# Kernel optimization log

Measured on AMD Instinct MI355X. Metric: run time of the kernel, lower is better.

Reference implementation:

```python
import jax, jax.numpy as jnp
import numpy as np

B, T, D, H = 4, 2048, 1024, 16
DH = D // H  # head dim = 64
FLOAT_MIN = jnp.finfo(jnp.float32).min


def setup_inputs() -> dict:
    key = jax.random.key(0)
    k1, k2, k3 = jax.random.split(key, 3)
    scale = 1.0 / np.sqrt(D)
    return {
        "x": jax.random.normal(k1, (B, T, D), dtype=jnp.float32),
        "W_qkv": jax.random.normal(k2, (D, 3 * D), dtype=jnp.float32) * scale,
        "b_qkv": jnp.zeros((3 * D,), dtype=jnp.float32),
        "W_out": jax.random.normal(k3, (D, D), dtype=jnp.float32) * scale,
        "b_out": jnp.zeros((D,), dtype=jnp.float32),
        "mask": jnp.ones((B, T, T), dtype=jnp.float32),
    }


def _split_heads(t):
    # [B, T, D] -> [B, H, T, DH]
    b, s, _ = t.shape
    return t.reshape(b, s, H, DH).transpose(0, 2, 1, 3)


def reference(x, W_qkv, b_qkv, W_out, b_out, mask):
    # fused QKV projection (Conv1D kernel-size 1 == per-position dense)
    qkv = jnp.einsum("btd,de->bte", x, W_qkv) + b_qkv
    q, k, v = jnp.split(qkv, 3, axis=-1)
    q = _split_heads(q) * (DH ** -0.5)  # [B, H, T, DH]
    k = _split_heads(k)
    v = _split_heads(v)
    # scores [B, H, Tq, Tk]
    dot = jnp.einsum("bhqd,bhkd->bhqk", q, k)
    m = mask[:, None, :, :]  # expand over heads
    dot = dot * m + (1.0 - m) * FLOAT_MIN
    attn = jax.nn.softmax(dot, axis=-1)
    ctx = jnp.einsum("bhqk,bhkd->bhqd", attn, v)  # [B, H, T, DH]
    combined = ctx.transpose(0, 2, 1, 3).reshape(x.shape[0], x.shape[1], D)
    out = jnp.einsum("btd,de->bte", combined, W_out) + b_out
    return out
```

## Files before the change

### kernel.cpp

```cpp
#include <hip/hip_runtime.h>

typedef short bf16x8 __attribute__((ext_vector_type(8)));
typedef float f32x4 __attribute__((ext_vector_type(4)));
typedef float f32x16 __attribute__((ext_vector_type(16)));
typedef unsigned short u16x8 __attribute__((ext_vector_type(8)));

#define DEVI __device__ __forceinline__

static constexpr int T_ = 2048;

DEVI unsigned short f2bf(float f) {
  unsigned int x = __builtin_bit_cast(unsigned int, f);
  x += 0x7fffu + ((x >> 16) & 1u);
  return (unsigned short)(x >> 16);
}

DEVI unsigned int cvtpk(float lo, float hi2) {
  unsigned int r;
  asm("v_cvt_pk_bf16_f32 %0, %1, %2" : "=v"(r) : "v"(lo), "v"(hi2));
  return r;
}

DEVI float exp2_raw(float x) {
  float r;
  asm("v_exp_f32 %0, %1" : "=v"(r) : "v"(x));
  return r;
}

DEVI int swz23(int r) {
  const int d = ((r >> 2) ^ (r >> 3)) & 1;
  return r ^ (d << 2) ^ (d << 3);
}

DEVI bf16x8 mkfrag(unsigned a, unsigned b, unsigned c, unsigned d) {
  union { unsigned u[4]; bf16x8 v; } x;
  x.u[0] = a; x.u[1] = b; x.u[2] = c; x.u[3] = d;
  return x.v;
}

DEVI void gl2lds16(const void* g, const void* l) {
  __builtin_amdgcn_global_load_lds(
      (const __attribute__((address_space(1))) void*)g,
      (__attribute__((address_space(3))) void*)l, 16, 0, 0);
}

__global__ __launch_bounds__(256) void k_cvt_bf16(const float* __restrict__ in,
                                                  unsigned short* __restrict__ out) {
  size_t i = ((size_t)blockIdx.x * 256 + threadIdx.x) * 8;
  float4 a = *(const float4*)(in + i);
  float4 b = *(const float4*)(in + i + 4);
  u16x8 o;
  o[0] = f2bf(a.x); o[1] = f2bf(a.y); o[2] = f2bf(a.z); o[3] = f2bf(a.w);
  o[4] = f2bf(b.x); o[5] = f2bf(b.y); o[6] = f2bf(b.z); o[7] = f2bf(b.w);
  *(u16x8*)(out + i) = o;
}

__global__ __launch_bounds__(256) void k_mask_scan(const uint4* __restrict__ m,
                                                   unsigned int* __restrict__ flag) {
  const unsigned int ONE = 0x3f800000u;
  size_t i0 = ((size_t)blockIdx.x * 256 + threadIdx.x) * 8;
  bool ok = true;
#pragma unroll
  for (int i = 0; i < 8; ++i) {
    uint4 v = m[i0 + i];
    ok &= (v.x == ONE) & (v.y == ONE) & (v.z == ONE) & (v.w == ONE);
  }
  if (!ok) atomicAnd(flag, 0u);
}

template <int R, int C>
__global__ __launch_bounds__(256) void k_transpose_cvt(const float* __restrict__ in,
                                                       unsigned short* __restrict__ out) {
  __shared__ unsigned short t[64][65];
  const int c0 = blockIdx.x * 64, r0 = blockIdx.y * 64;
  const int cc = threadIdx.x & 63, r4 = threadIdx.x >> 6;
#pragma unroll
  for (int i = 0; i < 16; ++i) {
    int rr = i * 4 + r4;
    t[rr][cc] = f2bf(in[(size_t)(r0 + rr) * C + c0 + cc]);
  }
  __syncthreads();
#pragma unroll
  for (int i = 0; i < 16; ++i) {
    int rr = i * 4 + r4;
    out[(size_t)(c0 + rr) * R + r0 + cc] = t[cc][rr];
  }
}

__global__ __launch_bounds__(256) void k_transpose_v(const unsigned short* __restrict__ V,
                                                     unsigned short* __restrict__ Vt) {
  __shared__ unsigned short t[64][65];
  const int t0 = blockIdx.x * 64;
  const size_t bh = blockIdx.y;
  const unsigned short* src = V + (bh * T_ + t0) * 64;
  unsigned short* dst = Vt + bh * 64 * T_ + t0;
  const int cc = threadIdx.x & 63, r4 = threadIdx.x >> 6;
#pragma unroll
  for (int i = 0; i < 16; ++i) {
    int rr = i * 4 + r4;
    t[rr][cc] = src[(size_t)rr * 64 + cc];
  }
  __syncthreads();
#pragma unroll
  for (int i = 0; i < 16; ++i) {
    int rr = i * 4 + r4;
    dst[(size_t)rr * T_ + cc] = t[cc][rr];
  }
}

template <int EPI>
__global__ __launch_bounds__(256, 3) void k_gemm(
    const unsigned short* __restrict__ A, const unsigned short* __restrict__ Bt,
    const float* __restrict__ bias,
    unsigned short* __restrict__ qo, unsigned short* __restrict__ ko2,
    unsigned short* __restrict__ vo, float* __restrict__ fo) {
  __shared__ unsigned short As[2][128 * 32];
  __shared__ unsigned short Bs[2][128 * 32];
  const int tid = threadIdx.x;
  const int lane = tid & 63, w = tid >> 6;
  const int wr = w >> 1, wc = w & 1;
  const int g = lane >> 4, c0 = lane & 15;
  const int m0 = blockIdx.y * 128, n0 = blockIdx.x * 128;

  f32x4 acc[4][4] = {};

  const int s0 = tid, s1 = tid + 256;
  const int ar0 = s0 >> 2, ac0 = (s0 & 3) ^ ((ar0 >> 1) & 3);
  const int ar1 = s1 >> 2, ac1 = (s1 & 3) ^ ((ar1 >> 1) & 3);
  const int ldsb0 = w * 512, ldsb1 = w * 512 + 2048;

  const unsigned short* Ar0 = A + (size_t)(m0 + ar0) * 1024 + ac0 * 8;
  const unsigned short* Ar1 = A + (size_t)(m0 + ar1) * 1024 + ac1 * 8;
  const unsigned short* Br0 = Bt + (size_t)(n0 + ar0) * 1024 + ac0 * 8;
  const unsigned short* Br1 = Bt + (size_t)(n0 + ar1) * 1024 + ac1 * 8;

  auto stage = [&](int buf, int kt) {
    const int ke = kt * 32;
    gl2lds16(Ar0 + ke, &As[buf][ldsb0]);
    gl2lds16(Ar1 + ke, &As[buf][ldsb1]);
    gl2lds16(Br0 + ke, &Bs[buf][ldsb0]);
    gl2lds16(Br1 + ke, &Bs[buf][ldsb1]);
  };

  stage(0, 0);
  __syncthreads();
  int cur = 0;
  for (int kt = 0; kt < 32; ++kt) {
    if (kt + 1 < 32) stage(cur ^ 1, kt + 1);
    bf16x8 af[4], bfv[4];
#pragma unroll
    for (int mf = 0; mf < 4; ++mf) {
      int row = wr * 64 + mf * 16 + c0;
      int ch = g ^ ((row >> 1) & 3);
      af[mf] = *(const bf16x8*)&As[cur][row * 32 + ch * 8];
    }
#pragma unroll
    for (int nf = 0; nf < 4; ++nf) {
      int row = wc * 64 + nf * 16 + c0;
      int ch = g ^ ((row >> 1) & 3);
      bfv[nf] = *(const bf16x8*)&Bs[cur][row * 32 + ch * 8];
    }
    __builtin_amdgcn_s_setprio(1);
#pragma unroll
    for (int mf = 0; mf < 4; ++mf)
#pragma unroll
      for (int nf = 0; nf < 4; ++nf)
        acc[mf][nf] = __builtin_amdgcn_mfma_f32_16x16x32_bf16(af[mf], bfv[nf], acc[mf][nf], 0, 0, 0);
    __builtin_amdgcn_s_setprio(0);
    __syncthreads();
    cur ^= 1;
  }

#pragma unroll
  for (int mf = 0; mf < 4; ++mf) {
#pragma unroll
    for (int nf = 0; nf < 4; ++nf) {
      const int n = n0 + wc * 64 + nf * 16 + c0;
      const float bv = bias[n];
#pragma unroll
      for (int r = 0; r < 4; ++r) {
        const int m = m0 + wr * 64 + mf * 16 + g * 4 + r;
        float v = acc[mf][nf][r] + bv;
        if constexpr (EPI == 0) {
          const int sel = n >> 10, hd = n & 1023;
          const int h = hd >> 6, d = hd & 63;
          const int b = m >> 11, t = m & 2047;
          const size_t off = ((size_t)((b * 16 + h) * 2048 + t)) * 64 + d;
          if (sel == 0)       qo[off] = f2bf(v * 0.125f);
          else if (sel == 1)  ko2[off] = f2bf(v);
          else                vo[off] = f2bf(v);
        } else {
          fo[(size_t)m * 1024 + n] = v;
        }
      }
    }
  }
}

__global__ __launch_bounds__(256, 4) void k_attn(
    const unsigned short* __restrict__ Q, const unsigned short* __restrict__ Kg_,
    const unsigned short* __restrict__ Vt, const float* __restrict__ mask,
    const unsigned int* __restrict__ maskflag,
    unsigned short* __restrict__ ctx) {
  __shared__ unsigned short Ks[2][64 * 64];
  __shared__ unsigned short Vs[2][64 * 64];
  const int tid = threadIdx.x, lane = tid & 63, w = tid >> 6;
  const int q = lane & 31, hi = lane >> 5;

  const int flat = blockIdx.x + 16 * blockIdx.y + 256 * blockIdx.z;
  const int work = (flat & 7) * 128 + (flat >> 3);
  const int qb = work & 15;
  const int bh_i = work >> 4;
  const int h = bh_i & 15, b = bh_i >> 4;
  const int t0 = qb * 128;
  const size_t bh = (size_t)bh_i;

  const unsigned short* Qg = Q + (bh * 2048 + t0 + w * 32 + q) * 64;
  const unsigned short* Kg = Kg_ + bh * 2048 * 64;
  const unsigned short* Vg = Vt + bh * 64 * 2048;
  const float* Mg = mask + (size_t)b * 2048 * 2048;
  const bool allones = (*maskflag != 0u);

  bf16x8 qf[4];
#pragma unroll
  for (int kd = 0; kd < 4; ++kd)
    qf[kd] = *(const bf16x8*)(Qg + kd * 16 + hi * 8);

  f32x16 ot[2] = {};
  float mrun = -__builtin_inff(), lrun = 0.f;

  const int s0 = tid, s1 = tid + 256;
  const int kr0 = s0 >> 3, kc0 = (s0 & 7) ^ (kr0 & 7);
  const int kr1 = s1 >> 3, kc1 = (s1 & 7) ^ (kr1 & 7);
  const int kp0 = swz23(kr0), kp1 = swz23(kr1);
  const int ldsb0 = w * 512, ldsb1 = w * 512 + 2048;

  auto stageKV = [&](int buf, int kt) {
    gl2lds16(Kg + (size_t)(kt * 64 + kp0) * 64 + kc0 * 8, &Ks[buf][ldsb0]);
    gl2lds16(Kg + (size_t)(kt * 64 + kp1) * 64 + kc1 * 8, &Ks[buf][ldsb1]);
    gl2lds16(Vg + (size_t)kr0 * 2048 + kt * 64 + kc0 * 8, &Vs[buf][ldsb0]);
    gl2lds16(Vg + (size_t)kr1 * 2048 + kt * 64 + kc1 * 8, &Vs[buf][ldsb1]);
  };

  stageKV(0, 0);
  __syncthreads();
  int cur = 0;
  const float MINF = -3.402823466e38f;
  const float L2E = 1.4426950408889634f;

  for (int kt = 0; kt < 32; ++kt) {
    if (kt + 1 < 32) stageKV(cur ^ 1, kt + 1);

    f32x16 st[2] = {};
#pragma unroll
    for (int mt2 = 0; mt2 < 2; ++mt2) {
      __builtin_amdgcn_s_setprio(1);
#pragma unroll
      for (int kd = 0; kd < 4; ++kd) {
        const int row = mt2 * 32 + q;
        const int ch = (2 * kd + hi) ^ (row & 7);
        bf16x8 kf = *(const bf16x8*)&Ks[cur][row * 64 + ch * 8];
        st[mt2] = __builtin_amdgcn_mfma_f32_32x32x16_bf16(kf, qf[kd], st[mt2], 0, 0, 0);
      }
      __builtin_amdgcn_s_setprio(0);
    }

    if (!allones) {
      const int qg = t0 + w * 32 + q;
#pragma unroll
      for (int mt2 = 0; mt2 < 2; ++mt2)
#pragma unroll
        for (int r = 0; r < 16; ++r) {
          const int kg = kt * 64 + mt2 * 32 +
                         (r & 3) + 4 * ((r >> 2) & 1) + 8 * hi + 16 * (r >> 3);
          const float mv = Mg[(size_t)qg * 2048 + kg];
          st[mt2][r] = st[mt2][r] * mv + (1.f - mv) * MINF;
        }
    }

    float g4[8];
#pragma unroll
    for (int i = 0; i < 4; ++i) {
      g4[i]     = fmaxf(fmaxf(fmaxf(st[0][4 * i], st[0][4 * i + 1]), st[0][4 * i + 2]), st[0][4 * i + 3]);
      g4[i + 4] = fmaxf(fmaxf(fmaxf(st[1][4 * i], st[1][4 * i + 1]), st[1][4 * i + 2]), st[1][4 * i + 3]);
    }
    float r1 = fmaxf(fmaxf(g4[0], g4[1]), g4[2]);
    float r2 = fmaxf(fmaxf(g4[3], g4[4]), g4[5]);
    float r3 = fmaxf(fmaxf(g4[6], g4[7]), r1);
    float tmax = fmaxf(r2, r3);
    tmax = fmaxf(tmax, __shfl_xor(tmax, 32));
    const bool defer = (__all(tmax <= mrun + 8.f) != 0);
    float alpha = 1.f;
    if (!defer) {
      const float mnew = fmaxf(mrun, tmax);
      alpha = exp2_raw((mrun - mnew) * L2E);
      mrun = mnew;
    }
    const float mL2 = mrun * L2E;
#pragma unroll
    for (int mt2 = 0; mt2 < 2; ++mt2)
#pragma unroll
      for (int i = 0; i < 16; ++i)
        st[mt2][i] = exp2_raw(st[mt2][i] * L2E - mL2);
    float s8[8];
#pragma unroll
    for (int i = 0; i < 8; ++i)
      s8[i] = (st[0][i] + st[0][i + 8]) + (st[1][i] + st[1][i + 8]);
    float s4a = s8[0] + s8[4], s4b = s8[1] + s8[5];
    float s4c = s8[2] + s8[6], s4d = s8[3] + s8[7];
    float ps = (s4a + s4b) + (s4c + s4d);
    ps += __shfl_xor(ps, 32);
    lrun = lrun * alpha + ps;
    if (!defer) {
#pragma unroll
      for (int dt = 0; dt < 2; ++dt)
#pragma unroll
        for (int i = 0; i < 16; ++i) ot[dt][i] *= alpha;
    }

    bf16x8 pf[4];
#pragma unroll
    for (int mt2 = 0; mt2 < 2; ++mt2) {
      unsigned int pw[8];
#pragma unroll
      for (int i = 0; i < 8; ++i) pw[i] = cvtpk(st[mt2][2 * i], st[mt2][2 * i + 1]);
      pf[2 * mt2]     = mkfrag(pw[0], pw[1], pw[2], pw[3]);
      pf[2 * mt2 + 1] = mkfrag(pw[4], pw[5], pw[6], pw[7]);
    }

#pragma unroll
    for (int dt = 0; dt < 2; ++dt) {
      __builtin_amdgcn_s_setprio(1);
#pragma unroll
      for (int kt2 = 0; kt2 < 4; ++kt2) {
        const int row = dt * 32 + q;
        const int ch = (2 * kt2 + hi) ^ (row & 7);
        bf16x8 vf = *(const bf16x8*)&Vs[cur][row * 64 + ch * 8];
        ot[dt] = __builtin_amdgcn_mfma_f32_32x32x16_bf16(vf, pf[kt2], ot[dt], 0, 0, 0);
      }
      __builtin_amdgcn_s_setprio(0);
    }

    __syncthreads();
    cur ^= 1;
  }

  const int qg = t0 + w * 32 + q;
  const float rl = 1.f / lrun;
  unsigned short* cp = ctx + ((size_t)b * 2048 + qg) * 1024 + h * 64;
#pragma unroll
  for (int dt = 0; dt < 2; ++dt) {
#pragma unroll
    for (int rg = 0; rg < 4; ++rg) {
      const int d0 = dt * 32 + rg * 8 + hi * 4;
      ushort4 o;
      o.x = f2bf(ot[dt][rg * 4 + 0] * rl);
      o.y = f2bf(ot[dt][rg * 4 + 1] * rl);
      o.z = f2bf(ot[dt][rg * 4 + 2] * rl);
      o.w = f2bf(ot[dt][rg * 4 + 3] * rl);
      *(ushort4*)(cp + d0) = o;
    }
  }
}

extern "C" void kernel_launch(void* const* d_in, const int* in_sizes, int n_in,
                              void* d_out, int out_size, void* d_ws, size_t ws_size,
                              hipStream_t stream) {
  (void)in_sizes; (void)n_in; (void)out_size; (void)ws_size;
  const float* x    = (const float*)d_in[0];
  const float* Wqkv = (const float*)d_in[1];
  const float* bqkv = (const float*)d_in[2];
  const float* Wout = (const float*)d_in[3];
  const float* bout = (const float*)d_in[4];
  const float* mask = (const float*)d_in[5];
  float* out = (float*)d_out;
  char* ws = (char*)d_ws;

  const size_t SZ_BTD = (size_t)8192 * 1024 * 2;
  unsigned short* xb  = (unsigned short*)(ws);
  unsigned short* Wqt = (unsigned short*)(ws + SZ_BTD);
  unsigned short* Wot = (unsigned short*)(ws + SZ_BTD + 6291456);
  unsigned short* Qb  = (unsigned short*)(ws + SZ_BTD + 8388608);
  unsigned short* Kb  = (unsigned short*)(ws + SZ_BTD + 8388608 + SZ_BTD);
  unsigned short* Vb  = (unsigned short*)(ws + SZ_BTD + 8388608 + 2 * SZ_BTD);
  unsigned short* Vtb = (unsigned short*)(ws + SZ_BTD + 8388608 + 3 * SZ_BTD);
  unsigned int* flag  = (unsigned int*)(ws + SZ_BTD + 8388608 + 4 * SZ_BTD);
  unsigned short* ctx = xb;

  hipMemsetAsync(flag, 1, 4, stream);
  k_mask_scan<<<2048, 256, 0, stream>>>((const uint4*)mask, flag);
  k_cvt_bf16<<<4096, 256, 0, stream>>>(x, xb);
  k_transpose_cvt<1024, 3072><<<dim3(48, 16), 256, 0, stream>>>(Wqkv, Wqt);
  k_transpose_cvt<1024, 1024><<<dim3(16, 16), 256, 0, stream>>>(Wout, Wot);
  k_gemm<0><<<dim3(24, 64), 256, 0, stream>>>(xb, Wqt, bqkv, Qb, Kb, Vb, nullptr);
  k_transpose_v<<<dim3(32, 64), 256, 0, stream>>>(Vb, Vtb);
  k_attn<<<dim3(16, 16, 4), 256, 0, stream>>>(Qb, Kb, Vtb, mask, flag, ctx);
  k_gemm<1><<<dim3(8, 64), 256, 0, stream>>>(ctx, Wot, bout, nullptr, nullptr, nullptr, out);
}
```

Baseline: 230.8 us.

## Process two query tiles per wave in attention to reuse K/V fragments

Each attention wave now handles 64 query rows, as two 32-row sub-tiles sharing every K and V fragment read from LDS. The block size grows to 256 queries and the grid shrinks to 512 blocks. Launch bounds are lowered to 2 blocks per CU to make room for the doubled accumulators. Separately, the GEMM drops its MFMA priority boosts and lowers its occupancy bound. The goal is to halve LDS reads and global K/V staging per query, at the cost of lower occupancy and fewer blocks across the CUs.

```diff
diff --git a/kernel.cpp b/kernel.cpp
--- a/kernel.cpp
+++ b/kernel.cpp
@@ -109,7 +109,7 @@
 }
 
 template <int EPI>
-__global__ __launch_bounds__(256, 3) void k_gemm(
+__global__ __launch_bounds__(256, 2) void k_gemm(
     const unsigned short* __restrict__ A, const unsigned short* __restrict__ Bt,
     const float* __restrict__ bias,
     unsigned short* __restrict__ qo, unsigned short* __restrict__ ko2,
@@ -160,13 +160,11 @@
       int ch = g ^ ((row >> 1) & 3);
       bfv[nf] = *(const bf16x8*)&Bs[cur][row * 32 + ch * 8];
     }
-    __builtin_amdgcn_s_setprio(1);
 #pragma unroll
     for (int mf = 0; mf < 4; ++mf)
 #pragma unroll
       for (int nf = 0; nf < 4; ++nf)
         acc[mf][nf] = __builtin_amdgcn_mfma_f32_16x16x32_bf16(af[mf], bfv[nf], acc[mf][nf], 0, 0, 0);
-    __builtin_amdgcn_s_setprio(0);
     __syncthreads();
     cur ^= 1;
   }
@@ -197,7 +195,7 @@
   }
 }
 
-__global__ __launch_bounds__(256, 4) void k_attn(
+__global__ __launch_bounds__(256, 2) void k_attn(
     const unsigned short* __restrict__ Q, const unsigned short* __restrict__ Kg_,
     const unsigned short* __restrict__ Vt, const float* __restrict__ mask,
     const unsigned int* __restrict__ maskflag,
@@ -207,27 +205,31 @@
   const int tid = threadIdx.x, lane = tid & 63, w = tid >> 6;
   const int q = lane & 31, hi = lane >> 5;
 
-  const int flat = blockIdx.x + 16 * blockIdx.y + 256 * blockIdx.z;
-  const int work = (flat & 7) * 128 + (flat >> 3);
-  const int qb = work & 15;
-  const int bh_i = work >> 4;
+  const int flat = blockIdx.x;
+  const int work = (flat & 7) * 64 + (flat >> 3);
+  const int qb = work & 7;
+  const int bh_i = work >> 3;
   const int h = bh_i & 15, b = bh_i >> 4;
-  const int t0 = qb * 128;
+  const int t0 = qb * 256;
   const size_t bh = (size_t)bh_i;
 
-  const unsigned short* Qg = Q + (bh * 2048 + t0 + w * 32 + q) * 64;
+  const unsigned short* Qg0 = Q + (bh * 2048 + t0 + w * 64 + q) * 64;
+  const unsigned short* Qg1 = Qg0 + 32 * 64;
   const unsigned short* Kg = Kg_ + bh * 2048 * 64;
   const unsigned short* Vg = Vt + bh * 64 * 2048;
   const float* Mg = mask + (size_t)b * 2048 * 2048;
   const bool allones = (*maskflag != 0u);
 
-  bf16x8 qf[4];
-#pragma unroll
-  for (int kd = 0; kd < 4; ++kd)
-    qf[kd] = *(const bf16x8*)(Qg + kd * 16 + hi * 8);
-
-  f32x16 ot[2] = {};
-  float mrun = -__builtin_inff(), lrun = 0.f;
+  bf16x8 qf0[4], qf1[4];
+#pragma unroll
+  for (int kd = 0; kd < 4; ++kd) {
+    qf0[kd] = *(const bf16x8*)(Qg0 + kd * 16 + hi * 8);
+    qf1[kd] = *(const bf16x8*)(Qg1 + kd * 16 + hi * 8);
+  }
+
+  f32x16 ot0[2] = {}, ot1[2] = {};
+  float mrun0 = -__builtin_inff(), lrun0 = 0.f;
+  float mrun1 = -__builtin_inff(), lrun1 = 0.f;
 
   const int s0 = tid, s1 = tid + 256;
   const int kr0 = s0 >> 3, kc0 = (s0 & 7) ^ (kr0 & 7);
@@ -248,36 +250,7 @@
   const float MINF = -3.402823466e38f;
   const float L2E = 1.4426950408889634f;
 
-  for (int kt = 0; kt < 32; ++kt) {
-    if (kt + 1 < 32) stageKV(cur ^ 1, kt + 1);
-
-    f32x16 st[2] = {};
-#pragma unroll
-    for (int mt2 = 0; mt2 < 2; ++mt2) {
-      __builtin_amdgcn_s_setprio(1);
-#pragma unroll
-      for (int kd = 0; kd < 4; ++kd) {
-        const int row = mt2 * 32 + q;
-        const int ch = (2 * kd + hi) ^ (row & 7);
-        bf16x8 kf = *(const bf16x8*)&Ks[cur][row * 64 + ch * 8];
-        st[mt2] = __builtin_amdgcn_mfma_f32_32x32x16_bf16(kf, qf[kd], st[mt2], 0, 0, 0);
-      }
-      __builtin_amdgcn_s_setprio(0);
-    }
-
-    if (!allones) {
-      const int qg = t0 + w * 32 + q;
-#pragma unroll
-      for (int mt2 = 0; mt2 < 2; ++mt2)
-#pragma unroll
-        for (int r = 0; r < 16; ++r) {
-          const int kg = kt * 64 + mt2 * 32 +
-                         (r & 3) + 4 * ((r >> 2) & 1) + 8 * hi + 16 * (r >> 3);
-          const float mv = Mg[(size_t)qg * 2048 + kg];
-          st[mt2][r] = st[mt2][r] * mv + (1.f - mv) * MINF;
-        }
-    }
-
+  auto softmax_pack = [&](f32x16* st, float& mrun, float& lrun, f32x16* ot, bf16x8* pf) {
     float g4[8];
 #pragma unroll
     for (int i = 0; i < 4; ++i) {
@@ -317,8 +290,6 @@
 #pragma unroll
         for (int i = 0; i < 16; ++i) ot[dt][i] *= alpha;
     }
-
-    bf16x8 pf[4];
 #pragma unroll
     for (int mt2 = 0; mt2 < 2; ++mt2) {
       unsigned int pw[8];
@@ -327,6 +298,44 @@
       pf[2 * mt2]     = mkfrag(pw[0], pw[1], pw[2], pw[3]);
       pf[2 * mt2 + 1] = mkfrag(pw[4], pw[5], pw[6], pw[7]);
     }
+  };
+
+  for (int kt = 0; kt < 32; ++kt) {
+    if (kt + 1 < 32) stageKV(cur ^ 1, kt + 1);
+
+    f32x16 st0[2] = {}, st1[2] = {};
+#pragma unroll
+    for (int mt2 = 0; mt2 < 2; ++mt2) {
+      __builtin_amdgcn_s_setprio(1);
+#pragma unroll
+      for (int kd = 0; kd < 4; ++kd) {
+        const int row = mt2 * 32 + q;
+        const int ch = (2 * kd + hi) ^ (row & 7);
+        bf16x8 kf = *(const bf16x8*)&Ks[cur][row * 64 + ch * 8];
+        st0[mt2] = __builtin_amdgcn_mfma_f32_32x32x16_bf16(kf, qf0[kd], st0[mt2], 0, 0, 0);
+        st1[mt2] = __builtin_amdgcn_mfma_f32_32x32x16_bf16(kf, qf1[kd], st1[mt2], 0, 0, 0);
+      }
+      __builtin_amdgcn_s_setprio(0);
+    }
+
+    if (!allones) {
+      const int qg0 = t0 + w * 64 + q;
+#pragma unroll
+      for (int mt2 = 0; mt2 < 2; ++mt2)
+#pragma unroll
+        for (int r = 0; r < 16; ++r) {
+          const int kg = kt * 64 + mt2 * 32 +
+                         (r & 3) + 4 * ((r >> 2) & 1) + 8 * hi + 16 * (r >> 3);
+          const float mv0 = Mg[(size_t)qg0 * 2048 + kg];
+          const float mv1 = Mg[(size_t)(qg0 + 32) * 2048 + kg];
+          st0[mt2][r] = st0[mt2][r] * mv0 + (1.f - mv0) * MINF;
+          st1[mt2][r] = st1[mt2][r] * mv1 + (1.f - mv1) * MINF;
+        }
+    }
+
+    bf16x8 pf0[4], pf1[4];
+    softmax_pack(st0, mrun0, lrun0, ot0, pf0);
+    softmax_pack(st1, mrun1, lrun1, ot1, pf1);
 
 #pragma unroll
     for (int dt = 0; dt < 2; ++dt) {
@@ -336,7 +345,8 @@
         const int row = dt * 32 + q;
         const int ch = (2 * kt2 + hi) ^ (row & 7);
         bf16x8 vf = *(const bf16x8*)&Vs[cur][row * 64 + ch * 8];
-        ot[dt] = __builtin_amdgcn_mfma_f32_32x32x16_bf16(vf, pf[kt2], ot[dt], 0, 0, 0);
+        ot0[dt] = __builtin_amdgcn_mfma_f32_32x32x16_bf16(vf, pf0[kt2], ot0[dt], 0, 0, 0);
+        ot1[dt] = __builtin_amdgcn_mfma_f32_32x32x16_bf16(vf, pf1[kt2], ot1[dt], 0, 0, 0);
       }
       __builtin_amdgcn_s_setprio(0);
     }
@@ -345,20 +355,26 @@
     cur ^= 1;
   }
 
-  const int qg = t0 + w * 32 + q;
-  const float rl = 1.f / lrun;
-  unsigned short* cp = ctx + ((size_t)b * 2048 + qg) * 1024 + h * 64;
+  const int qg0 = t0 + w * 64 + q;
+  const float rl0 = 1.f / lrun0, rl1 = 1.f / lrun1;
+  unsigned short* cp0 = ctx + ((size_t)b * 2048 + qg0) * 1024 + h * 64;
+  unsigned short* cp1 = cp0 + (size_t)32 * 1024;
 #pragma unroll
   for (int dt = 0; dt < 2; ++dt) {
 #pragma unroll
     for (int rg = 0; rg < 4; ++rg) {
       const int d0 = dt * 32 + rg * 8 + hi * 4;
-      ushort4 o;
-      o.x = f2bf(ot[dt][rg * 4 + 0] * rl);
-      o.y = f2bf(ot[dt][rg * 4 + 1] * rl);
-      o.z = f2bf(ot[dt][rg * 4 + 2] * rl);
-      o.w = f2bf(ot[dt][rg * 4 + 3] * rl);
-      *(ushort4*)(cp + d0) = o;
+      ushort4 o0, o1;
+      o0.x = f2bf(ot0[dt][rg * 4 + 0] * rl0);
+      o0.y = f2bf(ot0[dt][rg * 4 + 1] * rl0);
+      o0.z = f2bf(ot0[dt][rg * 4 + 2] * rl0);
+      o0.w = f2bf(ot0[dt][rg * 4 + 3] * rl0);
+      o1.x = f2bf(ot1[dt][rg * 4 + 0] * rl1);
+      o1.y = f2bf(ot1[dt][rg * 4 + 1] * rl1);
+      o1.z = f2bf(ot1[dt][rg * 4 + 2] * rl1);
+      o1.w = f2bf(ot1[dt][rg * 4 + 3] * rl1);
+      *(ushort4*)(cp0 + d0) = o0;
+      *(ushort4*)(cp1 + d0) = o1;
     }
   }
 }
@@ -394,6 +410,6 @@
   k_transpose_cvt<1024, 1024><<<dim3(16, 16), 256, 0, stream>>>(Wout, Wot);
   k_gemm<0><<<dim3(24, 64), 256, 0, stream>>>(xb, Wqt, bqkv, Qb, Kb, Vb, nullptr);
   k_transpose_v<<<dim3(32, 64), 256, 0, stream>>>(Vb, Vtb);
-  k_attn<<<dim3(16, 16, 4), 256, 0, stream>>>(Qb, Kb, Vtb, mask, flag, ctx);
+  k_attn<<<512, 256, 0, stream>>>(Qb, Kb, Vtb, mask, flag, ctx);
   k_gemm<1><<<dim3(8, 64), 256, 0, stream>>>(ctx, Wot, bout, nullptr, nullptr, nullptr, out);
 }
```

After: 239.9 us. 4.0% more time.

## Fuse V transpose into QKV GEMM epilogue and remap blocks across XCDs

Applied to the files above, without the earlier changes.

The QKV GEMM epilogue now writes V directly in transposed [B,H,DH,T] layout, so the separate V-transpose kernel and its intermediate buffer are removed. Block indices are remapped so consecutive blocks are spread across the 8 XCD chunks, which is meant to improve L2 locality. The change also drops the s_setprio hints around the MFMA loop and lowers the launch-bounds occupancy hint from 3 to 2. The transposed V stores are strided (2048 elements apart per d), so the epilogue writes become poorly coalesced.

```diff
diff --git a/kernel.cpp b/kernel.cpp
--- a/kernel.cpp
+++ b/kernel.cpp
@@ -87,40 +87,24 @@
   }
 }
 
-__global__ __launch_bounds__(256) void k_transpose_v(const unsigned short* __restrict__ V,
-                                                     unsigned short* __restrict__ Vt) {
-  __shared__ unsigned short t[64][65];
-  const int t0 = blockIdx.x * 64;
-  const size_t bh = blockIdx.y;
-  const unsigned short* src = V + (bh * T_ + t0) * 64;
-  unsigned short* dst = Vt + bh * 64 * T_ + t0;
-  const int cc = threadIdx.x & 63, r4 = threadIdx.x >> 6;
-#pragma unroll
-  for (int i = 0; i < 16; ++i) {
-    int rr = i * 4 + r4;
-    t[rr][cc] = src[(size_t)rr * 64 + cc];
-  }
-  __syncthreads();
-#pragma unroll
-  for (int i = 0; i < 16; ++i) {
-    int rr = i * 4 + r4;
-    dst[(size_t)rr * T_ + cc] = t[cc][rr];
-  }
-}
-
 template <int EPI>
-__global__ __launch_bounds__(256, 3) void k_gemm(
+__global__ __launch_bounds__(256, 2) void k_gemm(
     const unsigned short* __restrict__ A, const unsigned short* __restrict__ Bt,
     const float* __restrict__ bias,
     unsigned short* __restrict__ qo, unsigned short* __restrict__ ko2,
-    unsigned short* __restrict__ vo, float* __restrict__ fo) {
+    unsigned short* __restrict__ vt, float* __restrict__ fo) {
   __shared__ unsigned short As[2][128 * 32];
   __shared__ unsigned short Bs[2][128 * 32];
   const int tid = threadIdx.x;
   const int lane = tid & 63, w = tid >> 6;
   const int wr = w >> 1, wc = w & 1;
   const int g = lane >> 4, c0 = lane & 15;
-  const int m0 = blockIdx.y * 128, n0 = blockIdx.x * 128;
+
+  const int nx = gridDim.x;
+  const int flat = blockIdx.y * nx + blockIdx.x;
+  const int chunk = (nx * gridDim.y) >> 3;
+  const int work = (flat & 7) * chunk + (flat >> 3);
+  const int m0 = (work / nx) * 128, n0 = (work % nx) * 128;
 
   f32x4 acc[4][4] = {};
 
@@ -160,13 +144,11 @@
       int ch = g ^ ((row >> 1) & 3);
       bfv[nf] = *(const bf16x8*)&Bs[cur][row * 32 + ch * 8];
     }
-    __builtin_amdgcn_s_setprio(1);
 #pragma unroll
     for (int mf = 0; mf < 4; ++mf)
 #pragma unroll
       for (int nf = 0; nf < 4; ++nf)
         acc[mf][nf] = __builtin_amdgcn_mfma_f32_16x16x32_bf16(af[mf], bfv[nf], acc[mf][nf], 0, 0, 0);
-    __builtin_amdgcn_s_setprio(0);
     __syncthreads();
     cur ^= 1;
   }
@@ -185,10 +167,10 @@
           const int sel = n >> 10, hd = n & 1023;
           const int h = hd >> 6, d = hd & 63;
           const int b = m >> 11, t = m & 2047;
-          const size_t off = ((size_t)((b * 16 + h) * 2048 + t)) * 64 + d;
-          if (sel == 0)       qo[off] = f2bf(v * 0.125f);
-          else if (sel == 1)  ko2[off] = f2bf(v);
-          else                vo[off] = f2bf(v);
+          const size_t bh = (size_t)(b * 16 + h);
+          if (sel == 0)       qo[(bh * 2048 + t) * 64 + d] = f2bf(v * 0.125f);
+          else if (sel == 1)  ko2[(bh * 2048 + t) * 64 + d] = f2bf(v);
+          else                vt[(bh * 64 + d) * 2048 + t] = f2bf(v);
         } else {
           fo[(size_t)m * 1024 + n] = v;
         }
@@ -382,9 +364,8 @@
   unsigned short* Wot = (unsigned short*)(ws + SZ_BTD + 6291456);
   unsigned short* Qb  = (unsigned short*)(ws + SZ_BTD + 8388608);
   unsigned short* Kb  = (unsigned short*)(ws + SZ_BTD + 8388608 + SZ_BTD);
-  unsigned short* Vb  = (unsigned short*)(ws + SZ_BTD + 8388608 + 2 * SZ_BTD);
-  unsigned short* Vtb = (unsigned short*)(ws + SZ_BTD + 8388608 + 3 * SZ_BTD);
-  unsigned int* flag  = (unsigned int*)(ws + SZ_BTD + 8388608 + 4 * SZ_BTD);
+  unsigned short* Vtb = (unsigned short*)(ws + SZ_BTD + 8388608 + 2 * SZ_BTD);
+  unsigned int* flag  = (unsigned int*)(ws + SZ_BTD + 8388608 + 3 * SZ_BTD);
   unsigned short* ctx = xb;
 
   hipMemsetAsync(flag, 1, 4, stream);
@@ -392,8 +373,7 @@
   k_cvt_bf16<<<4096, 256, 0, stream>>>(x, xb);
   k_transpose_cvt<1024, 3072><<<dim3(48, 16), 256, 0, stream>>>(Wqkv, Wqt);
   k_transpose_cvt<1024, 1024><<<dim3(16, 16), 256, 0, stream>>>(Wout, Wot);
-  k_gemm<0><<<dim3(24, 64), 256, 0, stream>>>(xb, Wqt, bqkv, Qb, Kb, Vb, nullptr);
-  k_transpose_v<<<dim3(32, 64), 256, 0, stream>>>(Vb, Vtb);
+  k_gemm<0><<<dim3(24, 64), 256, 0, stream>>>(xb, Wqt, bqkv, Qb, Kb, Vtb, nullptr);
   k_attn<<<dim3(16, 16, 4), 256, 0, stream>>>(Qb, Kb, Vtb, mask, flag, ctx);
   k_gemm<1><<<dim3(8, 64), 256, 0, stream>>>(ctx, Wot, bout, nullptr, nullptr, nullptr, out);
 }
```

After: 239.0 us. 1.04x slower.

## Rewrite GEMMs with 256x128 tiles, 8 waves, triple-buffered K=64 stages

Applied to the files above, without the earlier changes.

Replaces the 128x128, 4-wave, double-buffered GEMM with a 256x128 tile computed by 8 waves, K-step 64 and a three-deep LDS ring that prefetches two stages ahead under explicit vmcnt waits. A flattened grid remaps blocks so that consecutive workgroups land on different XCDs for better L2 locality. This aims to raise arithmetic intensity per LDS load and hide global latency better. In exchange it uses far more LDS (about 144KB per block), which limits occupancy and makes the hand-placed barrier and waitcnt sequencing fragile.

```diff
diff --git a/kernel.cpp b/kernel.cpp
--- a/kernel.cpp
+++ b/kernel.cpp
@@ -108,78 +108,98 @@
   }
 }
 
-template <int EPI>
-__global__ __launch_bounds__(256, 3) void k_gemm(
+template <int EPI, int NT>
+__global__ __launch_bounds__(512, 2) void k_gemm8(
     const unsigned short* __restrict__ A, const unsigned short* __restrict__ Bt,
     const float* __restrict__ bias,
     unsigned short* __restrict__ qo, unsigned short* __restrict__ ko2,
     unsigned short* __restrict__ vo, float* __restrict__ fo) {
-  __shared__ unsigned short As[2][128 * 32];
-  __shared__ unsigned short Bs[2][128 * 32];
-  const int tid = threadIdx.x;
-  const int lane = tid & 63, w = tid >> 6;
-  const int wr = w >> 1, wc = w & 1;
+  __shared__ unsigned short As[3][256 * 64];
+  __shared__ unsigned short Bs[3][128 * 64];
+  const int tid = threadIdx.x, lane = tid & 63, w = tid >> 6;
+  const int wm = w >> 1, wn = w & 1;
   const int g = lane >> 4, c0 = lane & 15;
-  const int m0 = blockIdx.y * 128, n0 = blockIdx.x * 128;
+
+  const int flat = blockIdx.x;
+  const int work = (flat & 7) * ((32 * NT) >> 3) + (flat >> 3);
+  const int m0 = (work / NT) * 256, n0 = (work % NT) * 128;
 
   f32x4 acc[4][4] = {};
 
-  const int s0 = tid, s1 = tid + 256;
-  const int ar0 = s0 >> 2, ac0 = (s0 & 3) ^ ((ar0 >> 1) & 3);
-  const int ar1 = s1 >> 2, ac1 = (s1 & 3) ^ ((ar1 >> 1) & 3);
-  const int ldsb0 = w * 512, ldsb1 = w * 512 + 2048;
-
-  const unsigned short* Ar0 = A + (size_t)(m0 + ar0) * 1024 + ac0 * 8;
-  const unsigned short* Ar1 = A + (size_t)(m0 + ar1) * 1024 + ac1 * 8;
-  const unsigned short* Br0 = Bt + (size_t)(n0 + ar0) * 1024 + ac0 * 8;
-  const unsigned short* Br1 = Bt + (size_t)(n0 + ar1) * 1024 + ac1 * 8;
-
-  auto stage = [&](int buf, int kt) {
-    const int ke = kt * 32;
-    gl2lds16(Ar0 + ke, &As[buf][ldsb0]);
-    gl2lds16(Ar1 + ke, &As[buf][ldsb1]);
-    gl2lds16(Br0 + ke, &Bs[buf][ldsb0]);
-    gl2lds16(Br1 + ke, &Bs[buf][ldsb1]);
+  const int rs = tid >> 3, chs = tid & 7;
+  const int lwb = w * 512;
+
+  auto stageK = [&](int buf, int kt) {
+    const unsigned short* sa = A + (size_t)m0 * 1024 + kt * 64;
+    const unsigned short* sb = Bt + (size_t)n0 * 1024 + kt * 64;
+    unsigned short* da = &As[buf][0];
+    unsigned short* db = &Bs[buf][0];
+#pragma unroll
+    for (int j = 0; j < 4; ++j) {
+      const int row = rs + j * 64;
+      const int ch = chs ^ (row & 7);
+      gl2lds16(sa + (size_t)row * 1024 + ch * 8, da + j * 4096 + lwb);
+    }
+#pragma unroll
+    for (int j = 0; j < 2; ++j) {
+      const int row = rs + j * 64;
+      const int ch = chs ^ (row & 7);
+      gl2lds16(sb + (size_t)row * 1024 + ch * 8, db + j * 4096 + lwb);
+    }
   };
 
-  stage(0, 0);
-  __syncthreads();
-  int cur = 0;
-  for (int kt = 0; kt < 32; ++kt) {
-    if (kt + 1 < 32) stage(cur ^ 1, kt + 1);
-    bf16x8 af[4], bfv[4];
+  stageK(0, 0);
+  stageK(1, 1);
+  asm volatile("s_waitcnt vmcnt(6)" ::: "memory");
+  __builtin_amdgcn_s_barrier();
+
+  int cb = 0;
+  for (int k = 0; k < 16; ++k) {
+    bf16x8 af[4][2], bfv[4][2];
 #pragma unroll
     for (int mf = 0; mf < 4; ++mf) {
-      int row = wr * 64 + mf * 16 + c0;
-      int ch = g ^ ((row >> 1) & 3);
-      af[mf] = *(const bf16x8*)&As[cur][row * 32 + ch * 8];
+      const int row = wm * 64 + mf * 16 + c0;
+#pragma unroll
+      for (int kk = 0; kk < 2; ++kk) {
+        const int ch = (kk * 4 + g) ^ (row & 7);
+        af[mf][kk] = *(const bf16x8*)&As[cb][row * 64 + ch * 8];
+      }
     }
 #pragma unroll
     for (int nf = 0; nf < 4; ++nf) {
-      int row = wc * 64 + nf * 16 + c0;
-      int ch = g ^ ((row >> 1) & 3);
-      bfv[nf] = *(const bf16x8*)&Bs[cur][row * 32 + ch * 8];
-    }
-    __builtin_amdgcn_s_setprio(1);
-#pragma unroll
-    for (int mf = 0; mf < 4; ++mf)
-#pragma unroll
-      for (int nf = 0; nf < 4; ++nf)
-        acc[mf][nf] = __builtin_amdgcn_mfma_f32_16x16x32_bf16(af[mf], bfv[nf], acc[mf][nf], 0, 0, 0);
-    __builtin_amdgcn_s_setprio(0);
-    __syncthreads();
-    cur ^= 1;
+      const int row = wn * 64 + nf * 16 + c0;
+#pragma unroll
+      for (int kk = 0; kk < 2; ++kk) {
+        const int ch = (kk * 4 + g) ^ (row & 7);
+        bfv[nf][kk] = *(const bf16x8*)&Bs[cb][row * 64 + ch * 8];
+      }
+    }
+    if (k + 2 < 16) stageK((cb + 2) % 3, k + 2);
+    __builtin_amdgcn_s_barrier();
+    asm volatile("s_waitcnt lgkmcnt(0)" ::: "memory");
+    __builtin_amdgcn_sched_barrier(0);
+#pragma unroll
+    for (int kk = 0; kk < 2; ++kk)
+#pragma unroll
+      for (int mf = 0; mf < 4; ++mf)
+#pragma unroll
+        for (int nf = 0; nf < 4; ++nf)
+          acc[mf][nf] = __builtin_amdgcn_mfma_f32_16x16x32_bf16(af[mf][kk], bfv[nf][kk], acc[mf][nf], 0, 0, 0);
+    if (k <= 13)      asm volatile("s_waitcnt vmcnt(6)" ::: "memory");
+    else if (k == 14) asm volatile("s_waitcnt vmcnt(0)" ::: "memory");
+    __builtin_amdgcn_s_barrier();
+    cb = (cb == 2) ? 0 : cb + 1;
   }
 
 #pragma unroll
   for (int mf = 0; mf < 4; ++mf) {
 #pragma unroll
     for (int nf = 0; nf < 4; ++nf) {
-      const int n = n0 + wc * 64 + nf * 16 + c0;
+      const int n = n0 + wn * 64 + nf * 16 + c0;
       const float bv = bias[n];
 #pragma unroll
       for (int r = 0; r < 4; ++r) {
-        const int m = m0 + wr * 64 + mf * 16 + g * 4 + r;
+        const int m = m0 + wm * 64 + mf * 16 + g * 4 + r;
         float v = acc[mf][nf][r] + bv;
         if constexpr (EPI == 0) {
           const int sel = n >> 10, hd = n & 1023;
@@ -392,8 +412,8 @@
   k_cvt_bf16<<<4096, 256, 0, stream>>>(x, xb);
   k_transpose_cvt<1024, 3072><<<dim3(48, 16), 256, 0, stream>>>(Wqkv, Wqt);
   k_transpose_cvt<1024, 1024><<<dim3(16, 16), 256, 0, stream>>>(Wout, Wot);
-  k_gemm<0><<<dim3(24, 64), 256, 0, stream>>>(xb, Wqt, bqkv, Qb, Kb, Vb, nullptr);
+  k_gemm8<0, 24><<<768, 512, 0, stream>>>(xb, Wqt, bqkv, Qb, Kb, Vb, nullptr);
   k_transpose_v<<<dim3(32, 64), 256, 0, stream>>>(Vb, Vtb);
   k_attn<<<dim3(16, 16, 4), 256, 0, stream>>>(Qb, Kb, Vtb, mask, flag, ctx);
-  k_gemm<1><<<dim3(8, 64), 256, 0, stream>>>(ctx, Wot, bout, nullptr, nullptr, nullptr, out);
-}
+  k_gemm8<1, 8><<<256, 512, 0, stream>>>(ctx, Wot, bout, nullptr, nullptr, nullptr, out);
+}
```

After: 223.7 us (median of 2 runs). -3.0%, faster.
